# Performance work log

Hardware: AMD Instinct MI355X
Metric: run time of the kernel (lower is better)

Reference implementation:

```python
import jax, jax.numpy as jnp
import numpy as np

EMBED_DIM = 1024
NUM_HEADS = 16
HEAD_DIM = EMBED_DIM // NUM_HEADS


def setup_inputs() -> dict:
    key = jax.random.key(0)
    ks = jax.random.split(key, 5)
    B, T, D = 4, 2048, EMBED_DIM
    s = 1.0 / np.sqrt(D)
    return {
        "x": jax.random.normal(ks[0], (B, T, D), dtype=jnp.float32),
        "qkv_w": jax.random.uniform(ks[1], (3 * D, D), jnp.float32, -s, s),
        "qkv_b": jax.random.uniform(ks[2], (3 * D,), jnp.float32, -s, s),
        "out_w": jax.random.uniform(ks[3], (D, D), jnp.float32, -s, s),
        "out_b": jax.random.uniform(ks[4], (D,), jnp.float32, -s, s),
    }


def reference(x, qkv_w, qkv_b, out_w, out_b):
    B, T, D = x.shape
    H, Hd = NUM_HEADS, HEAD_DIM
    qkv = x @ qkv_w.T + qkv_b                      # [B,T,3D]
    q, k, v = jnp.split(qkv, 3, axis=-1)
    def split_heads(t):
        return t.reshape(B, T, H, Hd).transpose(0, 2, 1, 3)  # [B,H,T,Hd]
    q, k, v = split_heads(q), split_heads(k), split_heads(v)
    scores = jnp.einsum("bhqd,bhkd->bhqk", q, k) / np.sqrt(Hd).astype(jnp.float32)
    w = jax.nn.softmax(scores, axis=-1)
    o = jnp.einsum("bhqk,bhkd->bhqd", w, v)        # [B,H,T,Hd]
    o = o.transpose(0, 2, 1, 3).reshape(B, T, D)
    return o @ out_w.T + out_b
```

## Files before the change

kernel.cpp:

```cpp
#include <hip/hip_runtime.h>
#include <stdint.h>


#define BD   4
#define TD   2048
#define DD   1024
#define HH   16
#define HDD  64
#define MM   8192

typedef __attribute__((ext_vector_type(8))) short  bf16x8;
typedef __attribute__((ext_vector_type(4))) float  f32x4;

typedef const __attribute__((address_space(1))) uint8_t gu8;
typedef __attribute__((address_space(3))) uint8_t       lu8;

__device__ __forceinline__ void async_copy16(const void* g, void* l) {
    __builtin_amdgcn_global_load_lds((gu8*)(uintptr_t)g, (lu8*)(uintptr_t)l, 16, 0, 0);
}

__device__ __forceinline__ ushort f2bf(float f) {
    uint32_t u = __float_as_uint(f);
    u += 0x7fffu + ((u >> 16) & 1u);
    return (ushort)(u >> 16);
}

__device__ __forceinline__ float fexp2(float x) {
#if __has_builtin(__builtin_amdgcn_exp2f)
    return __builtin_amdgcn_exp2f(x);
#else
    return __expf(x * 0.69314718056f);
#endif
}

__global__ __launch_bounds__(256) void castk3(const float* __restrict__ a, ushort* __restrict__ ao, int na4,
                                              const float* __restrict__ b, ushort* __restrict__ bo, int nb4,
                                              const float* __restrict__ c, ushort* __restrict__ co, int nc4) {
    const int stride = gridDim.x * blockDim.x;
    const int t0 = blockIdx.x * blockDim.x + threadIdx.x;
    for (int i = t0; i < na4; i += stride) {
        float4 v = ((const float4*)a)[i];
        ushort4 o; o.x = f2bf(v.x); o.y = f2bf(v.y); o.z = f2bf(v.z); o.w = f2bf(v.w);
        ((ushort4*)ao)[i] = o;
    }
    for (int i = t0; i < nb4; i += stride) {
        float4 v = ((const float4*)b)[i];
        ushort4 o; o.x = f2bf(v.x); o.y = f2bf(v.y); o.z = f2bf(v.z); o.w = f2bf(v.w);
        ((ushort4*)bo)[i] = o;
    }
    for (int i = t0; i < nc4; i += stride) {
        float4 v = ((const float4*)c)[i];
        ushort4 o; o.x = f2bf(v.x); o.y = f2bf(v.y); o.z = f2bf(v.z); o.w = f2bf(v.w);
        ((ushort4*)co)[i] = o;
    }
}

template <int MODE>
__global__ __launch_bounds__(256, 2) void gemm_bt(const ushort* __restrict__ A,
                                                  const ushort* __restrict__ W,
                                                  const float* __restrict__ bias,
                                                  float* __restrict__ outf,
                                                  ushort* __restrict__ qb,
                                                  ushort* __restrict__ kb,
                                                  ushort* __restrict__ vb,
                                                  int N) {
    constexpr int K = 1024;
    __shared__ ushort As[128 * 64];
    __shared__ ushort Bs[128 * 64];

    const int t    = threadIdx.x;
    const int lane = t & 63;
    const int wave = t >> 6;
    const int lg   = lane >> 4;
    const int l16  = lane & 15;
    const int wm   = wave >> 1;
    const int wn   = wave & 1;
    const int m0   = blockIdx.x * 128;
    const int n0   = blockIdx.y * 128;

    const int srow = t >> 3;
    const int scol = (t & 7) * 8;

    f32x4 acc[4][4] = {};

    for (int kt = 0; kt < K / 64; ++kt) {
        const ushort* Agp = A + (size_t)(m0 + srow) * K + kt * 64 + scol;
        const ushort* Wgp = W + (size_t)(n0 + srow) * K + kt * 64 + scol;
#pragma unroll
        for (int i = 0; i < 4; ++i) {
            async_copy16(Agp + (size_t)i * 32 * K, (char*)As + i * 4096 + t * 16);
            async_copy16(Wgp + (size_t)i * 32 * K, (char*)Bs + i * 4096 + t * 16);
        }
        __syncthreads();

#pragma unroll
        for (int kk = 0; kk < 2; ++kk) {
            bf16x8 af[4], bf[4];
#pragma unroll
            for (int m = 0; m < 4; ++m)
                af[m] = *(const bf16x8*)((const char*)As +
                        (wm * 64 + m * 16 + l16) * 128 + kk * 64 + lg * 16);
#pragma unroll
            for (int n = 0; n < 4; ++n)
                bf[n] = *(const bf16x8*)((const char*)Bs +
                        (wn * 64 + n * 16 + l16) * 128 + kk * 64 + lg * 16);
#pragma unroll
            for (int m = 0; m < 4; ++m)
#pragma unroll
                for (int n = 0; n < 4; ++n)
                    acc[m][n] = __builtin_amdgcn_mfma_f32_16x16x32_bf16(
                        af[m], bf[n], acc[m][n], 0, 0, 0);
        }
        __syncthreads();
    }

#pragma unroll
    for (int mf = 0; mf < 4; ++mf) {
#pragma unroll
        for (int nf = 0; nf < 4; ++nf) {
            f32x4 a = acc[mf][nf];
            const int n  = n0 + wn * 64 + nf * 16 + l16;
            const float bv = bias[n];
            if constexpr (MODE == 0) {
                const int which = n >> 10;
                const int dcol  = n & 1023;
                const int h  = dcol >> 6;
                const int hd = dcol & 63;
                const int mrow0 = m0 + wm * 64 + mf * 16 + lg * 4;
                const int b   = mrow0 >> 11;
                const int tt0 = mrow0 & 2047;
                if (which == 0) {
#pragma unroll
                    for (int r = 0; r < 4; ++r)
                        qb[(((size_t)(b * HH + h)) * TD + tt0 + r) * HDD + hd] =
                            f2bf((a[r] + bv) * 0.180336880f);
                } else if (which == 1) {
#pragma unroll
                    for (int r = 0; r < 4; ++r)
                        kb[(((size_t)(b * HH + h)) * TD + tt0 + r) * HDD + hd] =
                            f2bf(a[r] + bv);
                } else {
                    ushort4 pk;
                    pk.x = f2bf(a[0] + bv); pk.y = f2bf(a[1] + bv);
                    pk.z = f2bf(a[2] + bv); pk.w = f2bf(a[3] + bv);
                    *(ushort4*)(&vb[(((size_t)(b * HH + h)) * HDD + hd) * TD + tt0]) = pk;
                }
            } else {
#pragma unroll
                for (int r = 0; r < 4; ++r) {
                    const int m = m0 + wm * 64 + mf * 16 + lg * 4 + r;
                    outf[(size_t)m * N + n] = a[r] + bv;
                }
            }
        }
    }
}

__global__ __launch_bounds__(256, 3) void flash_attn(const ushort* __restrict__ Q,
                                                     const ushort* __restrict__ K,
                                                     const ushort* __restrict__ Vt,
                                                     ushort* __restrict__ O) {
    __shared__ char   Ks[2][8192];
    __shared__ char   Vs[2][8192];
    __shared__ ushort Pl[4][32 * 72];

    const int t    = threadIdx.x;
    const int lane = t & 63;
    const int wave = t >> 6;
    const int lg   = lane >> 4;
    const int l16  = lane & 15;

    const int lin  = blockIdx.y * 16 + blockIdx.x;
    const int work = (lin & 7) * 128 + (lin >> 3);
    const int bh   = work >> 4;
    const int q0   = (work & 15) * 128;

    const size_t base = (size_t)bh * TD * HDD;
    const ushort* Qp = Q  + base;
    const ushort* Kp = K  + base;
    const ushort* Vp = Vt + base;

    bf16x8 qf[2][2];
#pragma unroll
    for (int mf = 0; mf < 2; ++mf)
#pragma unroll
        for (int kk = 0; kk < 2; ++kk)
            qf[mf][kk] = *(const bf16x8*)(Qp +
                (q0 + wave * 32 + mf * 16 + l16) * HDD + kk * 32 + lg * 8);

    bf16x8 vone;
    {
        const short ov = (l16 == 0) ? (short)0x3F80 : (short)0;
        vone = bf16x8{ov, ov, ov, ov, ov, ov, ov, ov};
    }

    f32x4 o[2][4] = {};
    f32x4 osum[2] = {};

    const int sr = t >> 3;
    const int sc = ((t & 7) * 16) ^ ((sr & 7) << 4);
    const int ldst = t * 16;

#define STAGE(buf, kv)                                                         \
    do {                                                                       \
        const char* kg_ = (const char*)(Kp + (size_t)((kv) + sr) * HDD) + sc;  \
        async_copy16(kg_,                 &Ks[buf][0]    + ldst);              \
        async_copy16(kg_ + 32 * HDD * 2,  &Ks[buf][4096] + ldst);              \
        const char* vg_ = (const char*)(Vp + (size_t)sr * TD + (kv)) + sc;     \
        async_copy16(vg_,                 &Vs[buf][0]    + ldst);              \
        async_copy16(vg_ + 32 * TD * 2,   &Vs[buf][4096] + ldst);              \
    } while (0)

    STAGE(0, 0);
    int cur = 0;

    const int kxor = (l16 & 7) << 4;

    for (int kv0 = 0; kv0 < TD; kv0 += 64) {
        STAGE(cur ^ 1, (kv0 + 64) & (TD - 1));

        asm volatile("s_waitcnt vmcnt(4)" ::: "memory");
        asm volatile("s_barrier" ::: "memory");

        bf16x8 kf[2][4], vf[2][4];
#pragma unroll
        for (int kk = 0; kk < 2; ++kk)
#pragma unroll
            for (int nf = 0; nf < 4; ++nf)
                kf[kk][nf] = *(const bf16x8*)(&Ks[cur][(nf * 16 + l16) * 128 +
                                              ((kk * 64 + lg * 16) ^ kxor)]);
#pragma unroll
        for (int kk2 = 0; kk2 < 2; ++kk2)
#pragma unroll
            for (int df = 0; df < 4; ++df)
                vf[kk2][df] = *(const bf16x8*)(&Vs[cur][(df * 16 + l16) * 128 +
                                               ((kk2 * 64 + lg * 16) ^ kxor)]);

        f32x4 s[2][4] = {};
        __builtin_amdgcn_s_setprio(1);
#pragma unroll
        for (int kk = 0; kk < 2; ++kk)
#pragma unroll
            for (int mf = 0; mf < 2; ++mf)
#pragma unroll
                for (int nf = 0; nf < 4; ++nf)
                    s[mf][nf] = __builtin_amdgcn_mfma_f32_16x16x32_bf16(
                        qf[mf][kk], kf[kk][nf], s[mf][nf], 0, 0, 0);
        __builtin_amdgcn_s_setprio(0);

#pragma unroll
        for (int mf = 0; mf < 2; ++mf)
#pragma unroll
            for (int nf = 0; nf < 4; ++nf)
#pragma unroll
                for (int r = 0; r < 4; ++r)
                    Pl[wave][(mf * 16 + lg * 4 + r) * 72 + nf * 16 + l16] =
                        f2bf(fexp2(s[mf][nf][r]));

        __builtin_amdgcn_s_setprio(1);
#pragma unroll
        for (int kk2 = 0; kk2 < 2; ++kk2) {
            bf16x8 pf[2];
#pragma unroll
            for (int mf = 0; mf < 2; ++mf)
                pf[mf] = *(const bf16x8*)(&Pl[wave][(mf * 16 + l16) * 72 +
                                                    kk2 * 32 + lg * 8]);
#pragma unroll
            for (int mf = 0; mf < 2; ++mf) {
#pragma unroll
                for (int df = 0; df < 4; ++df)
                    o[mf][df] = __builtin_amdgcn_mfma_f32_16x16x32_bf16(
                        pf[mf], vf[kk2][df], o[mf][df], 0, 0, 0);
                osum[mf] = __builtin_amdgcn_mfma_f32_16x16x32_bf16(
                        pf[mf], vone, osum[mf], 0, 0, 0);
            }
        }
        __builtin_amdgcn_s_setprio(0);

        asm volatile("s_barrier" ::: "memory");
        cur ^= 1;
    }
#undef STAGE

    const int b = bh >> 4, h = bh & 15;
#pragma unroll
    for (int mf = 0; mf < 2; ++mf) {
#pragma unroll
        for (int r = 0; r < 4; ++r) {
            const float l   = __shfl(osum[mf][r], lane & 48);
            const float inv = 1.0f / l;
            const int tq = q0 + wave * 32 + mf * 16 + lg * 4 + r;
#pragma unroll
            for (int df = 0; df < 4; ++df)
                O[((size_t)(b * TD + tq)) * DD + h * HDD + df * 16 + l16] =
                    f2bf(o[mf][df][r] * inv);
        }
    }
}

extern "C" void kernel_launch(void* const* d_in, const int* in_sizes, int n_in,
                              void* d_out, int out_size, void* d_ws, size_t ws_size,
                              hipStream_t stream) {
    (void)in_sizes; (void)n_in; (void)out_size; (void)ws_size;

    const float* x     = (const float*)d_in[0];
    const float* qkv_w = (const float*)d_in[1];
    const float* qkv_b = (const float*)d_in[2];
    const float* out_w = (const float*)d_in[3];
    const float* out_b = (const float*)d_in[4];

    char* ws = (char*)d_ws;
    ushort* xb  = (ushort*)(ws);
    ushort* w1b = (ushort*)(ws + (16u << 20));
    ushort* w2b = (ushort*)(ws + (22u << 20));
    ushort* qb  = (ushort*)(ws + (24u << 20));
    ushort* kb  = (ushort*)(ws + (40u << 20));
    ushort* vb  = (ushort*)(ws + (56u << 20));
    ushort* ob  = (ushort*)(ws + (72u << 20));

    castk3<<<2048, 256, 0, stream>>>(x, xb, MM * DD / 4,
                                     qkv_w, w1b, 3 * DD * DD / 4,
                                     out_w, w2b, DD * DD / 4);

    gemm_bt<0><<<dim3(MM / 128, 3 * DD / 128), 256, 0, stream>>>(
        xb, w1b, qkv_b, nullptr, qb, kb, vb, 3 * DD);

    flash_attn<<<dim3(TD / 128, BD * HH), 256, 0, stream>>>(qb, kb, vb, ob);

    gemm_bt<1><<<dim3(MM / 128, DD / 128), 256, 0, stream>>>(
        ob, w2b, out_b, (float*)d_out, nullptr, nullptr, nullptr, DD);
}
```

Measured before the change: 276.0 us.

## Double flash-attention block to 512 threads and 256 queries with explicit scheduling barriers

Flash attention blocks now hold 8 waves covering 256 query rows, so each staged K/V tile is shared by twice as many waves. Each thread therefore issues one async copy per tensor instead of two. Explicit waitcnt and sched_barrier fences are added around LDS reads and the P round-trip, and the P fragments are hoisted out of the PV loop. The cost is fewer blocks in the grid, and the tighter fences may reduce overlap between memory and math.

```diff
diff --git a/kernel.cpp b/kernel.cpp
--- a/kernel.cpp
+++ b/kernel.cpp
@@ -156,13 +156,13 @@
     }
 }
 
-__global__ __launch_bounds__(256, 3) void flash_attn(const ushort* __restrict__ Q,
+__global__ __launch_bounds__(512, 4) void flash_attn(const ushort* __restrict__ Q,
                                                      const ushort* __restrict__ K,
                                                      const ushort* __restrict__ Vt,
                                                      ushort* __restrict__ O) {
     __shared__ char   Ks[2][8192];
     __shared__ char   Vs[2][8192];
-    __shared__ ushort Pl[4][32 * 72];
+    __shared__ ushort Pl[8][32 * 72];
 
     const int t    = threadIdx.x;
     const int lane = t & 63;
@@ -170,10 +170,10 @@
     const int lg   = lane >> 4;
     const int l16  = lane & 15;
 
-    const int lin  = blockIdx.y * 16 + blockIdx.x;
-    const int work = (lin & 7) * 128 + (lin >> 3);
-    const int bh   = work >> 4;
-    const int q0   = (work & 15) * 128;
+    const int lin  = blockIdx.y * 8 + blockIdx.x;
+    const int work = (lin & 7) * 64 + (lin >> 3);
+    const int bh   = work >> 3;
+    const int q0   = (work & 7) * 256;
 
     const size_t base = (size_t)bh * TD * HDD;
     const ushort* Qp = Q  + base;
@@ -203,12 +203,10 @@
 
 #define STAGE(buf, kv)                                                         \
     do {                                                                       \
-        const char* kg_ = (const char*)(Kp + (size_t)((kv) + sr) * HDD) + sc;  \
-        async_copy16(kg_,                 &Ks[buf][0]    + ldst);              \
-        async_copy16(kg_ + 32 * HDD * 2,  &Ks[buf][4096] + ldst);              \
-        const char* vg_ = (const char*)(Vp + (size_t)sr * TD + (kv)) + sc;     \
-        async_copy16(vg_,                 &Vs[buf][0]    + ldst);              \
-        async_copy16(vg_ + 32 * TD * 2,   &Vs[buf][4096] + ldst);              \
+        async_copy16((const char*)(Kp + (size_t)((kv) + sr) * HDD) + sc,       \
+                     &Ks[buf][0] + ldst);                                      \
+        async_copy16((const char*)(Vp + (size_t)sr * TD + (kv)) + sc,          \
+                     &Vs[buf][0] + ldst);                                      \
     } while (0)
 
     STAGE(0, 0);
@@ -219,8 +217,10 @@
     for (int kv0 = 0; kv0 < TD; kv0 += 64) {
         STAGE(cur ^ 1, (kv0 + 64) & (TD - 1));
 
-        asm volatile("s_waitcnt vmcnt(4)" ::: "memory");
+        asm volatile("s_waitcnt vmcnt(2)" ::: "memory");
+        __builtin_amdgcn_sched_barrier(0);
         asm volatile("s_barrier" ::: "memory");
+        __builtin_amdgcn_sched_barrier(0);
 
         bf16x8 kf[2][4], vf[2][4];
 #pragma unroll
@@ -235,6 +235,8 @@
             for (int df = 0; df < 4; ++df)
                 vf[kk2][df] = *(const bf16x8*)(&Vs[cur][(df * 16 + l16) * 128 +
                                                ((kk2 * 64 + lg * 16) ^ kxor)]);
+        asm volatile("s_waitcnt lgkmcnt(0)" ::: "memory");
+        __builtin_amdgcn_sched_barrier(0);
 
         f32x4 s[2][4] = {};
         __builtin_amdgcn_s_setprio(1);
@@ -256,28 +258,36 @@
                 for (int r = 0; r < 4; ++r)
                     Pl[wave][(mf * 16 + lg * 4 + r) * 72 + nf * 16 + l16] =
                         f2bf(fexp2(s[mf][nf][r]));
+        asm volatile("s_waitcnt lgkmcnt(0)" ::: "memory");
+        __builtin_amdgcn_sched_barrier(0);
+
+        bf16x8 pf[2][2];
+#pragma unroll
+        for (int kk2 = 0; kk2 < 2; ++kk2)
+#pragma unroll
+            for (int mf = 0; mf < 2; ++mf)
+                pf[kk2][mf] = *(const bf16x8*)(&Pl[wave][(mf * 16 + l16) * 72 +
+                                                         kk2 * 32 + lg * 8]);
+        asm volatile("s_waitcnt lgkmcnt(0)" ::: "memory");
+        __builtin_amdgcn_sched_barrier(0);
 
         __builtin_amdgcn_s_setprio(1);
 #pragma unroll
-        for (int kk2 = 0; kk2 < 2; ++kk2) {
-            bf16x8 pf[2];
-#pragma unroll
-            for (int mf = 0; mf < 2; ++mf)
-                pf[mf] = *(const bf16x8*)(&Pl[wave][(mf * 16 + l16) * 72 +
-                                                    kk2 * 32 + lg * 8]);
+        for (int kk2 = 0; kk2 < 2; ++kk2)
 #pragma unroll
             for (int mf = 0; mf < 2; ++mf) {
 #pragma unroll
                 for (int df = 0; df < 4; ++df)
                     o[mf][df] = __builtin_amdgcn_mfma_f32_16x16x32_bf16(
-                        pf[mf], vf[kk2][df], o[mf][df], 0, 0, 0);
+                        pf[kk2][mf], vf[kk2][df], o[mf][df], 0, 0, 0);
                 osum[mf] = __builtin_amdgcn_mfma_f32_16x16x32_bf16(
-                        pf[mf], vone, osum[mf], 0, 0, 0);
+                        pf[kk2][mf], vone, osum[mf], 0, 0, 0);
             }
-        }
         __builtin_amdgcn_s_setprio(0);
 
+        __builtin_amdgcn_sched_barrier(0);
         asm volatile("s_barrier" ::: "memory");
+        __builtin_amdgcn_sched_barrier(0);
         cur ^= 1;
     }
 #undef STAGE
@@ -325,7 +335,7 @@
     gemm_bt<0><<<dim3(MM / 128, 3 * DD / 128), 256, 0, stream>>>(
         xb, w1b, qkv_b, nullptr, qb, kb, vb, 3 * DD);
 
-    flash_attn<<<dim3(TD / 128, BD * HH), 256, 0, stream>>>(qb, kb, vb, ob);
+    flash_attn<<<dim3(TD / 256, BD * HH), 512, 0, stream>>>(qb, kb, vb, ob);
 
     gemm_bt<1><<<dim3(MM / 128, DD / 128), 256, 0, stream>>>(
         ob, w2b, out_b, (float*)d_out, nullptr, nullptr, nullptr, DD);
```

Measured after the change: 586.6 us. 2.13x slower.
